# Optimization experiments

Hardware: AMD Instinct MI355X
Metric: run time of the kernel (lower is better)

The kernel has to match this reference:

```python
import jax, jax.numpy as jnp
import numpy as np

B, M, D, H = 8, 1024, 512, 8


def setup_inputs() -> dict:
    key = jax.random.key(0)
    ks = jax.random.split(key, 8)
    s = 0.02
    return {
        'x': jax.random.normal(ks[0], (B, M, D), jnp.float32),
        'scale': jnp.ones((M, D), jnp.float32),
        'Wq': jax.random.normal(ks[1], (H, D, D), jnp.float32) * s,
        'Wk': jax.random.normal(ks[2], (H, D, D), jnp.float32) * s,
        'Wv': jax.random.normal(ks[3], (H, D, D), jnp.float32) * s,
        'Wo': jax.random.normal(ks[4], (D, H * D), jnp.float32) * s,
        'bo': jnp.zeros((D,), jnp.float32),
        'Wff': jax.random.normal(ks[5], (D, D), jnp.float32) * s,
        'bff': jnp.zeros((D,), jnp.float32),
        'Wg': jax.random.normal(ks[6], (D, D), jnp.float32) * s,
        'bg': jnp.zeros((D,), jnp.float32),
        'Wl': jax.random.normal(ks[7], (D, D), jnp.float32) * s,
        'bl': jnp.zeros((D,), jnp.float32),
        'beta': jnp.ones((1,), jnp.float32),
    }


def _rope_cos_sin(m, d):
    # theta = 10000 ** (-2*(i-1)/d), faithful to the original (note the i-1 quirk)
    i = jnp.arange(d // 2, dtype=jnp.float32)
    theta = jnp.power(10000.0, -2.0 * (i - 1.0) / d)
    ang = jnp.arange(m, dtype=jnp.float32)[:, None] * theta[None, :]  # [m, d/2]
    return jnp.cos(ang), jnp.sin(ang)


def _apply_rope(t, cos, sin):
    # t: [..., m, d]; equivalent to bmm with the block-diagonal rotation matrix R[p]
    te, to = t[..., 0::2], t[..., 1::2]
    re = te * cos + to * sin
    ro = -te * sin + to * cos
    return jnp.stack([re, ro], axis=-1).reshape(t.shape)


def _rmsnorm(x, scale):
    b, m, d = x.shape
    ff_rms = jnp.sqrt(jnp.sum(x * x, axis=(1, 2))) * (m * d) ** (-0.5)  # [b]
    return scale[None, :m, :] * (x / ff_rms[:, None, None])


def reference(x, scale, Wq, Wk, Wv, Wo, bo, Wff, bff, Wg, bg, Wl, bl, beta):
    b, m, d = x.shape
    xn = _rmsnorm(x, scale)

    # per-head full-width projections (nn.Linear: y = x @ W.T)
    q = jnp.einsum('bmd,hod->hbmo', xn, Wq)  # [H,B,M,D]
    k = jnp.einsum('bmd,hod->hbmo', xn, Wk)
    v = jnp.einsum('bmd,hod->hbmo', xn, Wv)

    cos, sin = _rope_cos_sin(m, d)
    qr = _apply_rope(q, cos, sin)
    kr = _apply_rope(k, cos, sin)

    # SDPA with is_causal=False (no mask); dropout disabled (eval)
    scores = jnp.einsum('hbqd,hbkd->hbqk', qr, kr) / jnp.sqrt(jnp.float32(d))
    attn = jax.nn.softmax(scores, axis=-1)
    ctx = jnp.einsum('hbqk,hbkd->hbqd', attn, v)  # [H,B,M,D]

    cat = jnp.transpose(ctx, (1, 2, 0, 3)).reshape(b, m, -1)  # [B,M,H*D]
    attn_out = cat @ Wo.T + bo

    x2 = xn + attn_out
    x3 = _rmsnorm(x2, scale)

    h1 = x3 @ Wff.T + bff
    g = h1 @ Wg.T + bg
    sw = g * jax.nn.sigmoid(beta * g)
    ff = sw * (h1 @ Wl.T + bl)
    return x3 + ff
```

## Files before the change

kernel.cpp:

```cpp
#include <hip/hip_runtime.h>
#include <math.h>

typedef unsigned short u16;
typedef float f32x2 __attribute__((ext_vector_type(2)));
typedef float f32x4 __attribute__((ext_vector_type(4)));
typedef __bf16 bf16x8 __attribute__((ext_vector_type(8)));
typedef unsigned short u16x4 __attribute__((ext_vector_type(4)));
typedef unsigned short u16x8 __attribute__((ext_vector_type(8)));

__device__ __forceinline__ float bf2f(u16 u) {
    union { float f; unsigned int i; } v; v.i = ((unsigned int)u) << 16; return v.f;
}
__device__ __forceinline__ u16 f2bf(float f) {
    union { float f; unsigned int i; } v; v.f = f;
    unsigned int r = v.i + 0x7fffu + ((v.i >> 16) & 1u);
    return (u16)(r >> 16);
}
__device__ __forceinline__ float dpp_swap1(float v) {
    union { float f; int i; } a, b; a.f = v;
    b.i = __builtin_amdgcn_update_dpp(0, a.i, 0xB1, 0xF, 0xF, true);
    return b.f;
}

__device__ __forceinline__ void gll(const u16* g, u16* l) {
    __builtin_amdgcn_global_load_lds((const __attribute__((address_space(1))) void*)g,
                                     (__attribute__((address_space(3))) void*)l, 16, 0, 0);
}

struct EpiBF16 {
    u16* C; long zs; int ldc;
    __device__ void operator()(int z, int m, int n, float v) const {
        C[(long)z * zs + (long)m * ldc + n] = f2bf(v);
    }
};
struct EpiScale {
    u16* C; long zs; int ldc; float s;
    __device__ void operator()(int z, int m, int n, float v) const {
        C[(long)z * zs + (long)m * ldc + n] = f2bf(v * s);
    }
};
struct EpiAcc {
    float* x2;
    __device__ void operator()(int z, int m, int n, float v) const {
        x2[(long)m * 512 + n] += v;
    }
};
struct EpiBias16 {
    u16* C; const float* bias;
    __device__ void operator()(int z, int m, int n, float v) const {
        C[(long)m * 512 + n] = f2bf(v + bias[n]);
    }
};
struct EpiGL {
    u16* g; u16* l; const float* bg; const float* bl;
    __device__ void operator()(int z, int m, int n, float v) const {
        if (n < 512) g[(long)m * 512 + n] = f2bf(v + bg[n]);
        else         l[(long)m * 512 + n - 512] = f2bf(v + bl[n - 512]);
    }
};
struct EpiCtxMul {
    u16* C; const float* rs;
    __device__ void operator()(int z, int m, int n, float v) const {
        float r = __builtin_amdgcn_rcpf(rs[(long)z * 1024 + m]);
        C[(long)z * 524288 + (long)m * 512 + n] = f2bf(v * r);
    }
};

struct EpiScores {
    u16* C; float* rs; float sscale;
    __device__ float elem(int z, int m, int n, float v) const {
        float e = __expf(v * sscale);
        C[(long)z * 1048576 + (long)m * 1024 + n] = f2bf(e);
        return e;
    }
    __device__ void row(int z, int m, float p, int l15) const {
        p += __shfl_xor(p, 1, 64); p += __shfl_xor(p, 2, 64);
        p += __shfl_xor(p, 4, 64); p += __shfl_xor(p, 8, 64);
        if (l15 == 0) atomicAdd(rs + (long)z * 1024 + m, p);
    }
};
struct EpiPart {
    float* p;
    __device__ float elem(int z, int m, int n, float v) const {
        p[(long)z * 4194304 + (long)m * 512 + n] = v;
        return 0.f;
    }
    __device__ void row(int, int, float, int) const {}
};

#define RDA(S, I) (*(const bf16x8*)(lds + (S) * 8192 + (I) * 512 + aro))
#define RDB(S, J) (*(const bf16x8*)(lds + (S) * 8192 + (J) * 512 + bro))
#define MFMA_PH(JP) do { \
    __builtin_amdgcn_s_barrier(); \
    asm volatile("s_waitcnt lgkmcnt(0)" ::: "memory"); \
    __builtin_amdgcn_sched_barrier(0); \
    __builtin_amdgcn_s_setprio(1); \
    _Pragma("unroll") \
    for (int i_ = 0; i_ < 8; i_++) { \
        acc[i_][2*(JP)]   = __builtin_amdgcn_mfma_f32_16x16x32_bf16(aF[i_], bF[0], acc[i_][2*(JP)], 0, 0, 0); \
        acc[i_][2*(JP)+1] = __builtin_amdgcn_mfma_f32_16x16x32_bf16(aF[i_], bF[1], acc[i_][2*(JP)+1], 0, 0, 0); \
    } \
    __builtin_amdgcn_s_setprio(0); \
} while (0)

__launch_bounds__(512, 2)
__global__ void gemm256_qkv(const u16* __restrict__ xnb, const u16* __restrict__ Wqkv,
                            u16* __restrict__ q, u16* __restrict__ k, u16* __restrict__ vT,
                            const float* __restrict__ csT) {
    __shared__ __align__(16) u16 lds[65536];
    const int t = threadIdx.x;
    const int lane = t & 63, wave = t >> 6;
    const int wr = wave >> 2, wc = wave & 3;
    const int l15 = lane & 15, quad = lane >> 4;
    const int sr = t >> 2;
    const int scw = ((t & 3) ^ ((t >> 3) & 3)) * 8;
    u16* lA0 = lds + wave * 512 + lane * 8;
    u16* lB0 = lds + 32768 + wave * 512 + lane * 8;
    const int ap = (quad ^ ((l15 >> 1) & 3)) * 8;
    const int aro = (wr * 128 + l15) * 32 + ap;
    const int bro = 32768 + (wc * 64 + l15) * 32 + ap;
    const int bid = blockIdx.x;

    const u16 *curA, *curB, *nxtA, *nxtB;
    int cm0, cn0, cz, cmode, nm0, nn0, nz, nmode;
    auto decode = [&](int tid, const u16*& A_, const u16*& B_,
                      int& m0_, int& n0_, int& z_, int& md_) {
        if (tid > 1535) tid = 1535;
        if (tid < 1024) {
            md_ = 0; z_ = tid & 15; int rem = tid >> 4;
            m0_ = (rem >> 1) << 8; n0_ = (rem & 1) << 8;
            A_ = xnb + (long)(m0_ + sr) * 512 + scw;
            B_ = Wqkv + z_ * 262144 + (long)(n0_ + sr) * 512 + scw;
        } else {
            int v = tid - 1024; md_ = 1; z_ = v & 7; int rem = v >> 3;
            m0_ = (rem & 1) << 8; n0_ = (rem >> 1) << 8;
            A_ = Wqkv + 4194304 + z_ * 262144 + (long)(m0_ + sr) * 512 + scw;
            B_ = xnb + (long)(n0_ + sr) * 512 + scw;
        }
    };
    decode(bid, curA, curB, cm0, cn0, cz, cmode);
    decode(bid + 256, nxtA, nxtB, nm0, nn0, nz, nmode);

    auto STGA = [&](int s) {
        const u16* base = (s < 16) ? curA : nxtA;
        int c = (s < 16) ? s : s - 16;
        u16* d = lA0 + (s & 3) * 8192;
        const u16* src = base + c * 32;
        gll(src, d); gll(src + 65536, d + 4096);
    };
    auto STGB = [&](int s) {
        const u16* base = (s < 16) ? curB : nxtB;
        int c = (s < 16) ? s : s - 16;
        u16* d = lB0 + (s & 3) * 8192;
        const u16* src = base + c * 32;
        gll(src, d); gll(src + 65536, d + 4096);
    };

    STGA(0); STGB(0); STGA(1); STGB(1); STGA(2); STGB(2);
    asm volatile("s_waitcnt vmcnt(4)" ::: "memory");
    __builtin_amdgcn_s_barrier();

    for (int j = 0; j < 6; ++j) {
        f32x4 acc[8][4] = {};
        #pragma unroll
        for (int it = 0; it < 4; ++it) {
            const int sh = 3 + it * 4;
            bf16x8 aF[8], bF[2];
            #pragma unroll
            for (int i = 0; i < 8; i++) aF[i] = RDA(0, i);
            bF[0] = RDB(0, 0); bF[1] = RDB(0, 1);
            STGA(sh);
            MFMA_PH(0);
            __builtin_amdgcn_s_barrier();
            bF[0] = RDB(0, 2); bF[1] = RDB(0, 3);
            STGB(sh);
            MFMA_PH(1);
            __builtin_amdgcn_s_barrier();
            #pragma unroll
            for (int i = 0; i < 8; i++) aF[i] = RDA(1, i);
            bF[0] = RDB(1, 0); bF[1] = RDB(1, 1);
            STGA(sh + 1);
            MFMA_PH(0);
            __builtin_amdgcn_s_barrier();
            bF[0] = RDB(1, 2); bF[1] = RDB(1, 3);
            STGB(sh + 1);
            MFMA_PH(1);
            asm volatile("s_waitcnt vmcnt(4)" ::: "memory");
            __builtin_amdgcn_s_barrier();
            #pragma unroll
            for (int i = 0; i < 8; i++) aF[i] = RDA(2, i);
            bF[0] = RDB(2, 0); bF[1] = RDB(2, 1);
            STGA(sh + 2);
            MFMA_PH(0);
            __builtin_amdgcn_s_barrier();
            bF[0] = RDB(2, 2); bF[1] = RDB(2, 3);
            STGB(sh + 2);
            MFMA_PH(1);
            __builtin_amdgcn_s_barrier();
            #pragma unroll
            for (int i = 0; i < 8; i++) aF[i] = RDA(3, i);
            bF[0] = RDB(3, 0); bF[1] = RDB(3, 1);
            STGA(sh + 3);
            MFMA_PH(0);
            __builtin_amdgcn_s_barrier();
            bF[0] = RDB(3, 2); bF[1] = RDB(3, 3);
            STGB(sh + 3);
            MFMA_PH(1);
            asm volatile("s_waitcnt vmcnt(4)" ::: "memory");
            __builtin_amdgcn_s_barrier();
        }
        if (cmode == 0) {
            u16* dst = ((cz >= 8) ? k : q) + ((long)(cz & 7) << 22);
            const int odd = l15 & 1;
            #pragma unroll
            for (int i = 0; i < 8; i++)
                #pragma unroll
                for (int r = 0; r < 4; r++) {
                    int m = cm0 + wr * 128 + i * 16 + quad * 4 + r;
                    const float* cs = csT + (long)(m & 1023) * 512;
                    #pragma unroll
                    for (int jj = 0; jj < 4; jj++) {
                        int n = cn0 + wc * 64 + jj * 16 + l15;
                        float val = acc[i][jj][r];
                        float pv = dpp_swap1(val);
                        float c = cs[(n >> 1) * 2], s = cs[(n >> 1) * 2 + 1];
                        float o = odd ? (val * c - pv * s) : (val * c + pv * s);
                        dst[(long)m * 512 + n] = f2bf(o);
                    }
                }
        } else {
            #pragma unroll
            for (int i = 0; i < 8; i++)
                #pragma unroll
                for (int r = 0; r < 4; r++) {
                    int m = cm0 + wr * 128 + i * 16 + quad * 4 + r;
                    #pragma unroll
                    for (int jj = 0; jj < 4; jj++) {
                        int n = cn0 + wc * 64 + jj * 16 + l15;
                        vT[((long)cz << 22) + ((long)(n >> 10) << 19) + ((long)m << 10) + (n & 1023)]
                            = f2bf(acc[i][jj][r]);
                    }
                }
        }
        curA = nxtA; curB = nxtB; cm0 = nm0; cn0 = nn0; cz = nz; cmode = nmode;
        decode(bid + (j + 2) * 256, nxtA, nxtB, nm0, nn0, nz, nmode);
    }
    asm volatile("s_waitcnt vmcnt(0)" ::: "memory");
}

template <class Epi>
__launch_bounds__(512, 2)
__global__ void gemm256(const u16* __restrict__ A, const u16* __restrict__ B,
                        int nkh, int kssh, int lda, int ldb,
                        long aBatch, long bBatch, long aSeg, long bSeg, Epi epi) {
    __shared__ __align__(16) u16 lds[65536];
    const int t = threadIdx.x;
    const int lane = t & 63, wave = t >> 6;
    const int wr = wave >> 2, wc = wave & 3;
    const int l15 = lane & 15, quad = lane >> 4;
    const int m0 = blockIdx.x * 256, n0 = blockIdx.y * 256;
    const int z = blockIdx.z;
    const int sr = t >> 2;
    const int scw = ((t & 3) ^ ((t >> 3) & 3)) * 8;
    const u16* gA = A + (long)z * aBatch + (long)(m0 + sr) * lda + scw;
    const u16* gB = B + (long)z * bBatch + (long)(n0 + sr) * ldb + scw;
    const long a128 = 128L * lda, b128 = 128L * ldb;
    u16* lA0 = lds + wave * 512 + lane * 8;
    u16* lB0 = lds + 32768 + wave * 512 + lane * 8;
    const int kmask = (1 << kssh) - 1;

    auto STA = [&](int shp) {
        int c = shp < nkh ? shp : nkh - 1;
        const u16* s = gA + (long)(c >> kssh) * aSeg + (c & kmask) * 32;
        u16* d = lA0 + (shp & 3) * 8192;
        gll(s, d); gll(s + a128, d + 4096);
    };
    auto STB = [&](int shp) {
        int c = shp < nkh ? shp : nkh - 1;
        const u16* s = gB + (long)(c >> kssh) * bSeg + (c & kmask) * 32;
        u16* d = lB0 + (shp & 3) * 8192;
        gll(s, d); gll(s + b128, d + 4096);
    };

    const int ap = (quad ^ ((l15 >> 1) & 3)) * 8;
    const int aro = (wr * 128 + l15) * 32 + ap;
    const int bro = 32768 + (wc * 64 + l15) * 32 + ap;
    f32x4 acc[8][4] = {};

    STA(0); STB(0); STA(1); STB(1); STA(2); STB(2);
    asm volatile("s_waitcnt vmcnt(4)" ::: "memory");
    __builtin_amdgcn_s_barrier();

    const int niter = nkh >> 2;
    int sh = 3;
    for (int it = 0; it < niter; it++) {
        bf16x8 aF[8], bF[2];
        #pragma unroll
        for (int i = 0; i < 8; i++) aF[i] = RDA(0, i);
        bF[0] = RDB(0, 0); bF[1] = RDB(0, 1);
        STA(sh);
        MFMA_PH(0);
        __builtin_amdgcn_s_barrier();
        bF[0] = RDB(0, 2); bF[1] = RDB(0, 3);
        STB(sh);
        MFMA_PH(1);
        __builtin_amdgcn_s_barrier();
        #pragma unroll
        for (int i = 0; i < 8; i++) aF[i] = RDA(1, i);
        bF[0] = RDB(1, 0); bF[1] = RDB(1, 1);
        STA(sh + 1);
        MFMA_PH(0);
        __builtin_amdgcn_s_barrier();
        bF[0] = RDB(1, 2); bF[1] = RDB(1, 3);
        STB(sh + 1);
        MFMA_PH(1);
        asm volatile("s_waitcnt vmcnt(4)" ::: "memory");
        __builtin_amdgcn_s_barrier();
        #pragma unroll
        for (int i = 0; i < 8; i++) aF[i] = RDA(2, i);
        bF[0] = RDB(2, 0); bF[1] = RDB(2, 1);
        STA(sh + 2);
        MFMA_PH(0);
        __builtin_amdgcn_s_barrier();
        bF[0] = RDB(2, 2); bF[1] = RDB(2, 3);
        STB(sh + 2);
        MFMA_PH(1);
        __builtin_amdgcn_s_barrier();
        #pragma unroll
        for (int i = 0; i < 8; i++) aF[i] = RDA(3, i);
        bF[0] = RDB(3, 0); bF[1] = RDB(3, 1);
        STA(sh + 3);
        MFMA_PH(0);
        __builtin_amdgcn_s_barrier();
        bF[0] = RDB(3, 2); bF[1] = RDB(3, 3);
        STB(sh + 3);
        MFMA_PH(1);
        asm volatile("s_waitcnt vmcnt(4)" ::: "memory");
        __builtin_amdgcn_s_barrier();
        sh += 4;
    }
    asm volatile("s_waitcnt vmcnt(0)" ::: "memory");

    #pragma unroll
    for (int i = 0; i < 8; i++)
        #pragma unroll
        for (int r = 0; r < 4; r++) {
            int m = m0 + wr * 128 + i * 16 + quad * 4 + r;
            float p = 0.f;
            #pragma unroll
            for (int j = 0; j < 4; j++)
                p += epi.elem(z, m, n0 + wc * 64 + j * 16 + l15, acc[i][j][r]);
            epi.row(z, m, p, l15);
        }
}
#undef RDA
#undef RDB
#undef MFMA_PH

template <class Epi>
__launch_bounds__(256, 4)
__global__ void gemm128(const u16* __restrict__ A, const u16* __restrict__ B,
                        int Kseg, int nSeg, int lda, int ldb,
                        long aBatch, long bBatch, long aSeg, Epi epi) {
    __shared__ __align__(16) u16 sA[8192];
    __shared__ __align__(16) u16 sB[8192];
    const int t = threadIdx.x;
    const int lane = t & 63, wave = t >> 6;
    const int wr = wave >> 1, wc = wave & 1;
    const int l15 = lane & 15, quad = lane >> 4;
    const int m0 = blockIdx.x * 128, n0 = blockIdx.y * 128;
    const int sr = t >> 2;
    const int scw = ((t & 3) ^ ((t >> 3) & 3)) * 8;
    const u16* gA = A + (long)blockIdx.z * aBatch + (long)(m0 + sr) * lda + scw;
    const u16* gB = B + (long)blockIdx.z * bBatch + (long)(n0 + sr) * ldb + scw;
    const long a2 = 64L * lda, b2 = 64L * ldb;
    u16* lA = sA + wave * 512 + lane * 8;
    u16* lB = sB + wave * 512 + lane * 8;
    const int ap = (quad ^ ((l15 >> 1) & 3)) * 8;
    const int ab = (wr * 64 + l15) * 32 + ap;
    const int bb = (wc * 64 + l15) * 32 + ap;
    f32x4 acc[4][4] = {};
    for (int s = 0; s < nSeg; s++) {
        const u16* gAs = gA + (long)s * aSeg;
        const u16* gBs = gB + s * Kseg;
        for (int k0 = 0; k0 < Kseg; k0 += 64) {
            gll(gAs + k0, lA);             gll(gAs + k0 + a2, lA + 2048);
            gll(gBs + k0, lB);             gll(gBs + k0 + b2, lB + 2048);
            gll(gAs + k0 + 32, lA + 4096); gll(gAs + k0 + 32 + a2, lA + 6144);
            gll(gBs + k0 + 32, lB + 4096); gll(gBs + k0 + 32 + b2, lB + 6144);
            __syncthreads();
            #pragma unroll
            for (int half = 0; half < 2; half++) {
                bf16x8 aF[4], bF[4];
                #pragma unroll
                for (int i = 0; i < 4; i++) aF[i] = *(const bf16x8*)(sA + half * 4096 + ab + i * 512);
                #pragma unroll
                for (int j = 0; j < 4; j++) bF[j] = *(const bf16x8*)(sB + half * 4096 + bb + j * 512);
                #pragma unroll
                for (int i = 0; i < 4; i++)
                    #pragma unroll
                    for (int j = 0; j < 4; j++)
                        acc[i][j] = __builtin_amdgcn_mfma_f32_16x16x32_bf16(aF[i], bF[j], acc[i][j], 0, 0, 0);
            }
            __syncthreads();
        }
    }
    #pragma unroll
    for (int i = 0; i < 4; i++)
        #pragma unroll
        for (int j = 0; j < 4; j++)
            #pragma unroll
            for (int r = 0; r < 4; r++)
                epi(blockIdx.z, m0 + wr * 64 + i * 16 + quad * 4 + r,
                    n0 + wc * 64 + j * 16 + l15, acc[i][j][r]);
}

__device__ __forceinline__ float waveSum(float v) {
    #pragma unroll
    for (int o = 32; o > 0; o >>= 1) v += __shfl_down(v, o, 64);
    return v;
}
__device__ __forceinline__ float invFromPart(const float* part, int b) {
    float s = part[b * 64 + (threadIdx.x & 63)];
    s = waveSum(s);
    s = __shfl(s, 0, 64);
    return sqrtf(524288.0f / s);
}

__global__ void sumsq_f32(const float* __restrict__ x, float* __restrict__ part) {
    __shared__ float tmp[4];
    long base = (long)blockIdx.x * 524288 + (long)blockIdx.y * 8192;
    float s = 0.f;
    for (int i = threadIdx.x * 4; i < 8192; i += 1024) {
        f32x4 v = *(const f32x4*)(x + base + i);
        s += v[0] * v[0] + v[1] * v[1] + v[2] * v[2] + v[3] * v[3];
    }
    s = waveSum(s);
    if ((threadIdx.x & 63) == 0) tmp[threadIdx.x >> 6] = s;
    __syncthreads();
    if (threadIdx.x == 0) part[blockIdx.x * 64 + blockIdx.y] = tmp[0] + tmp[1] + tmp[2] + tmp[3];
}
__global__ void combine_x2(float* __restrict__ x2, const float* __restrict__ p,
                           float* __restrict__ part) {
    __shared__ float tmp[4];
    long base = (long)blockIdx.x * 524288 + (long)blockIdx.y * 8192;
    float s = 0.f;
    for (int i = threadIdx.x * 4; i < 8192; i += 1024) {
        f32x4 v = *(const f32x4*)(x2 + base + i);
        v = v + *(const f32x4*)(p + base + i);
        v = v + *(const f32x4*)(p + 4194304 + base + i);
        v = v + *(const f32x4*)(p + 8388608 + base + i);
        v = v + *(const f32x4*)(p + 12582912 + base + i);
        *(f32x4*)(x2 + base + i) = v;
        s += v[0] * v[0] + v[1] * v[1] + v[2] * v[2] + v[3] * v[3];
    }
    s = waveSum(s);
    if ((threadIdx.x & 63) == 0) tmp[threadIdx.x >> 6] = s;
    __syncthreads();
    if (threadIdx.x == 0) part[blockIdx.x * 64 + blockIdx.y] = tmp[0] + tmp[1] + tmp[2] + tmp[3];
}
__global__ void finalize_inv(const float* __restrict__ part, float* __restrict__ inv) {
    float s = part[blockIdx.x * 64 + threadIdx.x];
    s = waveSum(s);
    if (threadIdx.x == 0) inv[blockIdx.x] = sqrtf(524288.0f / s);
}
__global__ void rmsnorm1f_a(const float* __restrict__ x, const float* __restrict__ scale,
                            const float* __restrict__ part, const float* __restrict__ bo,
                            u16* __restrict__ xnb, float* __restrict__ x2) {
    long i = ((long)blockIdx.x * 256 + threadIdx.x) * 4;
    int b = (int)(i >> 19);
    float inv = invFromPart(part, b);
    f32x4 xv = *(const f32x4*)(x + i);
    f32x4 sv = *(const f32x4*)(scale + (int)(i & 524287));
    f32x4 bv = *(const f32x4*)(bo + (int)(i & 511));
    f32x4 v; u16x4 o;
    #pragma unroll
    for (int j = 0; j < 4; j++) { v[j] = xv[j] * inv * sv[j]; o[j] = f2bf(v[j]); }
    *(u16x4*)(xnb + i) = o;
    *(f32x4*)(x2 + i) = v + bv;
}
__global__ void rmsnorm2_a(const float* __restrict__ x2, const float* __restrict__ scale,
                           const float* __restrict__ part, u16* __restrict__ x3b) {
    long i = ((long)blockIdx.x * 256 + threadIdx.x) * 4;
    int b = (int)(i >> 19);
    float inv = invFromPart(part, b);
    f32x4 xv = *(const f32x4*)(x2 + i);
    f32x4 sv = *(const f32x4*)(scale + (int)(i & 524287));
    u16x4 o;
    #pragma unroll
    for (int j = 0; j < 4; j++) o[j] = f2bf(xv[j] * inv * sv[j]);
    *(u16x4*)(x3b + i) = o;
}
__global__ void final_out_a(const float* __restrict__ x2, const float* __restrict__ scale,
                            const float* __restrict__ part, const u16* __restrict__ g,
                            const u16* __restrict__ l, const float* __restrict__ beta,
                            float* __restrict__ out) {
    long i = ((long)blockIdx.x * 256 + threadIdx.x) * 4;
    int b = (int)(i >> 19);
    float inv2 = invFromPart(part, b);
    float bta = beta[0];
    f32x4 xv = *(const f32x4*)(x2 + i);
    f32x4 sv = *(const f32x4*)(scale + (int)(i & 524287));
    u16x4 gv4 = *(const u16x4*)(g + i);
    u16x4 lv4 = *(const u16x4*)(l + i);
    f32x4 o;
    #pragma unroll
    for (int j = 0; j < 4; j++) {
        float x3 = xv[j] * inv2 * sv[j];
        float gv = bf2f(gv4[j]), lv = bf2f(lv4[j]);
        float sw = gv / (1.0f + __expf(-bta * gv));
        o[j] = x3 + sw * lv;
    }
    *(f32x4*)(out + i) = o;
}
__global__ void rmsnorm1f(const float* __restrict__ x, const float* __restrict__ scale,
                          const float* __restrict__ inv, const float* __restrict__ bo,
                          u16* __restrict__ xnb, float* __restrict__ x2) {
    long i = (long)blockIdx.x * 256 + threadIdx.x;
    int b = (int)(i >> 19), md = (int)(i & 524287);
    float v = x[i] * inv[b] * scale[md];
    xnb[i] = f2bf(v);
    x2[i] = v + bo[i & 511];
}
__global__ void rmsnorm2(const float* __restrict__ x2, const float* __restrict__ scale,
                         const float* __restrict__ inv, u16* __restrict__ x3b) {
    long i = (long)blockIdx.x * 256 + threadIdx.x;
    int b = (int)(i >> 19), md = (int)(i & 524287);
    x3b[i] = f2bf(x2[i] * inv[b] * scale[md]);
}
__global__ void final_out(const float* __restrict__ x2, const float* __restrict__ scale,
                          const float* __restrict__ inv2, const u16* __restrict__ g,
                          const u16* __restrict__ l, const float* __restrict__ beta,
                          float* __restrict__ out) {
    long i = (long)blockIdx.x * 256 + threadIdx.x;
    int b = (int)(i >> 19), md = (int)(i & 524287);
    float x3 = x2[i] * inv2[b] * scale[md];
    float gv = bf2f(g[i]), lv = bf2f(l[i]);
    float bta = beta[0];
    float sw = gv / (1.0f + expf(-bta * gv));
    out[i] = x3 + sw * lv;
}
#define LOG2_10000F 13.287712379549449f
__global__ void rope_tables_a(float* __restrict__ csT, float* __restrict__ rowsum) {
    int i = blockIdx.x * 256 + threadIdx.x;
    int m = i >> 8, j = i & 255;
    float theta = exp2f(LOG2_10000F * (-2.0f * ((float)j - 1.0f) / 512.0f));
    float ang = (float)m * theta;
    csT[2 * i] = cosf(ang); csT[2 * i + 1] = sinf(ang);
    if (i < 65536) rowsum[i] = 0.f;
}
__global__ void rope_tables(float* __restrict__ cosT, float* __restrict__ sinT) {
    int i = blockIdx.x * 256 + threadIdx.x;
    int m = i >> 8, j = i & 255;
    float theta = exp2f(LOG2_10000F * (-2.0f * ((float)j - 1.0f) / 512.0f));
    float ang = (float)m * theta;
    cosT[i] = cosf(ang); sinT[i] = sinf(ang);
}
__global__ void rope_apply(u16* __restrict__ tq, const float* __restrict__ cosT,
                           const float* __restrict__ sinT) {
    long i = (long)blockIdx.x * 256 + threadIdx.x;
    int j = (int)(i & 255), m = (int)((i >> 8) & 1023);
    float c = cosT[m * 256 + j], s = sinT[m * 256 + j];
    long base = i * 2;
    float te = bf2f(tq[base]), to = bf2f(tq[base + 1]);
    tq[base]     = f2bf(te * c + to * s);
    tq[base + 1] = f2bf(-te * s + to * c);
}
__global__ void transpose_v(const u16* __restrict__ v, u16* __restrict__ vT) {
    __shared__ u16 tile[32][33];
    long zb = (long)blockIdx.z * 524288;
    int mo = blockIdx.x * 32, oo = blockIdx.y * 32;
    int tx = threadIdx.x & 31, ty = threadIdx.x >> 5;
    for (int r = ty; r < 32; r += 8) tile[r][tx] = v[zb + (long)(mo + r) * 512 + oo + tx];
    __syncthreads();
    for (int r = ty; r < 32; r += 8) vT[zb + (long)(oo + r) * 1024 + mo + tx] = tile[tx][r];
}
__launch_bounds__(256)
__global__ void softmax_rows4(u16* __restrict__ sc) {
    int row = blockIdx.x * 4 + (threadIdx.x >> 6);
    int lane = threadIdx.x & 63;
    u16* p = sc + (long)row * 1024 + lane * 16;
    float v[16]; float mx = -1e30f;
    #pragma unroll
    for (int i = 0; i < 16; i++) { v[i] = bf2f(p[i]); mx = fmaxf(mx, v[i]); }
    #pragma unroll
    for (int o = 32; o > 0; o >>= 1) mx = fmaxf(mx, __shfl_xor(mx, o, 64));
    float s = 0.f;
    #pragma unroll
    for (int i = 0; i < 16; i++) { v[i] = expf(v[i] - mx); s += v[i]; }
    #pragma unroll
    for (int o = 32; o > 0; o >>= 1) s += __shfl_xor(s, o, 64);
    float r = 1.0f / s;
    #pragma unroll
    for (int i = 0; i < 16; i++) p[i] = f2bf(v[i] * r);
}
__device__ __forceinline__ void cvt8(const float* __restrict__ s, u16* __restrict__ d) {
    f32x4 a = *(const f32x4*)s, b = *(const f32x4*)(s + 4);
    u16x8 o;
    o[0] = f2bf(a[0]); o[1] = f2bf(a[1]); o[2] = f2bf(a[2]); o[3] = f2bf(a[3]);
    o[4] = f2bf(b[0]); o[5] = f2bf(b[1]); o[6] = f2bf(b[2]); o[7] = f2bf(b[3]);
    *(u16x8*)d = o;
}
__global__ void prep_w(const float* __restrict__ Wq, const float* __restrict__ Wk,
                       const float* __restrict__ Wv, const float* __restrict__ Wo,
                       const float* __restrict__ Wff, const float* __restrict__ Wg,
                       const float* __restrict__ Wl,
                       u16* __restrict__ Wqkvb, u16* __restrict__ Wob,
                       u16* __restrict__ Wffb, u16* __restrict__ Wglb) {
    long i = ((long)blockIdx.x * 256 + threadIdx.x) * 8;
    if (i < 2097152)      cvt8(Wq + i, Wqkvb + i);
    else if (i < 4194304) cvt8(Wk + (i - 2097152), Wqkvb + i);
    else if (i < 6291456) cvt8(Wv + (i - 4194304), Wqkvb + i);
    else if (i < 8388608) cvt8(Wo + (i - 6291456), Wob + (i - 6291456));
    else if (i < 8650752) cvt8(Wff + (i - 8388608), Wffb + (i - 8388608));
    else if (i < 8912896) cvt8(Wg + (i - 8650752), Wglb + (i - 8650752));
    else                  cvt8(Wl + (i - 8912896), Wglb + 262144 + (i - 8912896));
}
__global__ void convert_f2b(const float* __restrict__ s, u16* __restrict__ d, int n) {
    int i = blockIdx.x * 256 + threadIdx.x;
    if (i < n) d[i] = f2bf(s[i]);
}
__global__ void convert3(const float* __restrict__ a, const float* __restrict__ b,
                         const float* __restrict__ c, u16* __restrict__ d) {
    int i = blockIdx.x * 256 + threadIdx.x;
    const float* s = (i < 262144) ? a : (i < 524288) ? b : c;
    d[i] = f2bf(s[i & 262143]);
}

#define MB 1048576L
extern "C" void kernel_launch(void* const* d_in, const int* in_sizes, int n_in,
                              void* d_out, int out_size, void* d_ws, size_t ws_size,
                              hipStream_t stream) {
    (void)in_sizes; (void)n_in; (void)out_size;
    const float* x    = (const float*)d_in[0];
    const float* scale= (const float*)d_in[1];
    const float* Wq   = (const float*)d_in[2];
    const float* Wk   = (const float*)d_in[3];
    const float* Wv   = (const float*)d_in[4];
    const float* Wo   = (const float*)d_in[5];
    const float* bo   = (const float*)d_in[6];
    const float* Wff  = (const float*)d_in[7];
    const float* bff  = (const float*)d_in[8];
    const float* Wg   = (const float*)d_in[9];
    const float* bg   = (const float*)d_in[10];
    const float* Wl   = (const float*)d_in[11];
    const float* bl   = (const float*)d_in[12];
    const float* beta = (const float*)d_in[13];
    float* out = (float*)d_out;
    char* ws = (char*)d_ws;
    const float sscale = 0.044194173824159216f;

    if (ws_size >= 260000000UL) {
        u16*   xnb   = (u16*)  (ws);
        u16*   q_all = (u16*)  (ws + 8*MB);
        u16*   k_all = (u16*)  (ws + 72*MB);
        u16*   vT_all= (u16*)  (ws + 136*MB);
        u16*   sc    = (u16*)  (ws + 200*MB);
        u16*   Wqkvb = (u16*)  (ws + 200*MB);
        u16*   Wob   = (u16*)  (ws + 232*MB);
        u16*   Wffb  = (u16*)  (ws + 236*MB);
        u16*   Wglb  = (u16*)  (ws + 236*MB + 524288L);
        float* csT   = (float*)(ws + 237*MB + 1572864L);
        float* rowsum= (float*)(ws + 239*MB + 1572864L);
        float* part  = (float*)(ws + 239*MB + 1835008L);
        float* x2    = out;
        float* wop   = (float*)k_all;
        u16* x3b = k_all; u16* h1 = k_all + 4194304; u16* g = k_all + 8388608; u16* l = k_all + 12582912;

        sumsq_f32<<<dim3(8, 64), 256, 0, stream>>>(x, part);
        rmsnorm1f_a<<<4096, 256, 0, stream>>>(x, scale, part, bo, xnb, x2);
        rope_tables_a<<<1024, 256, 0, stream>>>(csT, rowsum);
        prep_w<<<4480, 256, 0, stream>>>(Wq, Wk, Wv, Wo, Wff, Wg, Wl,
                                         Wqkvb, Wob, Wffb, Wglb);

        gemm256_qkv<<<256, 512, 0, stream>>>(xnb, Wqkvb, q_all, k_all, vT_all, csT);

        for (int h0 = 0; h0 < 8; h0 += 2) {
            const long off = (long)h0 * 4194304;
            float* rsc = rowsum + (long)h0 * 8192;
            gemm256<<<dim3(4, 4, 16), 512, 0, stream>>>(q_all + off, k_all + off, 16, 4, 512, 512,
                524288L, 524288L, 512L, 512L, EpiScores{sc, rsc, sscale});
            gemm128<<<dim3(8, 4, 16), 256, 0, stream>>>(sc, vT_all + off, 1024, 1, 1024, 1024,
                1048576L, 524288L, 0L, EpiCtxMul{q_all + off, rsc});
        }
        gemm256<<<dim3(32, 2, 4), 512, 0, stream>>>(q_all, Wob, 32, 4, 512, 4096,
            8388608L, 1024L, 4194304L, 512L, EpiPart{wop});
        combine_x2<<<dim3(8, 64), 256, 0, stream>>>(x2, wop, part);
        rmsnorm2_a<<<4096, 256, 0, stream>>>(x2, scale, part, x3b);

        gemm128<<<dim3(64, 4, 1), 256, 0, stream>>>(x3b, Wffb, 512, 1, 512, 512,
            0L, 0L, 0L, EpiBias16{h1, bff});
        gemm128<<<dim3(64, 8, 1), 256, 0, stream>>>(h1, Wglb, 512, 1, 512, 512,
            0L, 0L, 0L, EpiGL{g, l, bg, bl});
        final_out_a<<<4096, 256, 0, stream>>>(x2, scale, part, g, l, beta, out);
        return;
    }

    u16*   xnb  = (u16*)  (ws);
    float* x2   = (float*)(ws + 8388608L);
    u16*   qh   = (u16*)  (ws + 25165824L);
    u16*   kh   = (u16*)  (ws + 33554432L);
    u16*   vhc  = (u16*)  (ws + 41943040L);
    u16*   vT   = (u16*)  (ws + 50331648L);
    u16*   Whb  = (u16*)  (ws + 58720256L);
    u16*   Wob  = (u16*)  (ws + 60293120L);
    u16*   Wfb  = (u16*)  (ws + 64487424L);
    u16*   Wgb  = (u16*)  (ws + 65011712L);
    u16*   Wlb  = (u16*)  (ws + 65536000L);
    float* cosT = (float*)(ws + 66060288L);
    float* sinT = (float*)(ws + 67108864L);
    float* part = (float*)(ws + 68157440L);
    float* inv1 = (float*)(ws + 68159488L);
    float* inv2 = (float*)(ws + 68159552L);
    u16*   sc   = (u16*)  (ws + 68159616L);
    u16*   x3b = qh;  u16* h1 = kh;  u16* g = vhc;  u16* l = vT;
    const bool big = ws_size >= 85002240UL;

    sumsq_f32<<<dim3(8, 64), 256, 0, stream>>>(x, part);
    finalize_inv<<<8, 64, 0, stream>>>(part, inv1);
    rmsnorm1f<<<16384, 256, 0, stream>>>(x, scale, inv1, bo, xnb, x2);
    rope_tables<<<1024, 256, 0, stream>>>(cosT, sinT);
    convert_f2b<<<8192, 256, 0, stream>>>(Wo, Wob, 2097152);
    convert_f2b<<<1024, 256, 0, stream>>>(Wff, Wfb, 262144);
    convert_f2b<<<1024, 256, 0, stream>>>(Wg, Wgb, 262144);
    convert_f2b<<<1024, 256, 0, stream>>>(Wl, Wlb, 262144);

    for (int h = 0; h < 8; h++) {
        convert3<<<3072, 256, 0, stream>>>(Wq + (long)h * 262144, Wk + (long)h * 262144,
                                           Wv + (long)h * 262144, Whb);
        gemm128<<<dim3(64, 4, 3), 256, 0, stream>>>(xnb, Whb, 512, 1, 512, 512, 0L, 262144L, 0L,
                                                    EpiBF16{qh, 4194304L, 512});
        rope_apply<<<16384, 256, 0, stream>>>(qh, cosT, sinT);
        transpose_v<<<dim3(32, 16, 8), 256, 0, stream>>>(vhc, vT);
        if (big) {
            gemm128<<<dim3(8, 8, 8), 256, 0, stream>>>(qh, kh, 512, 1, 512, 512, 524288L, 524288L,
                                                       0L, EpiScale{sc, 1048576L, 1024, sscale});
            softmax_rows4<<<2048, 256, 0, stream>>>(sc);
            gemm128<<<dim3(8, 4, 8), 256, 0, stream>>>(sc, vT, 1024, 1, 1024, 1024, 1048576L,
                                                       524288L, 0L, EpiBF16{vhc, 524288L, 512});
        } else {
            for (int b = 0; b < 8; b++) {
                gemm128<<<dim3(8, 8, 1), 256, 0, stream>>>(qh + (long)b * 524288, kh + (long)b * 524288,
                                                           512, 1, 512, 512, 0L, 0L, 0L,
                                                           EpiScale{sc, 0L, 1024, sscale});
                softmax_rows4<<<256, 256, 0, stream>>>(sc);
                gemm128<<<dim3(8, 4, 1), 256, 0, stream>>>(sc, vT + (long)b * 524288, 1024, 1, 1024,
                                                           1024, 0L, 0L, 0L,
                                                           EpiBF16{vhc + (long)b * 524288, 0L, 512});
            }
        }
        gemm128<<<dim3(64, 4, 1), 256, 0, stream>>>(vhc, Wob + (long)h * 512, 512, 1, 512, 4096,
                                                    0L, 0L, 0L, EpiAcc{x2});
    }

    sumsq_f32<<<dim3(8, 64), 256, 0, stream>>>(x2, part);
    finalize_inv<<<8, 64, 0, stream>>>(part, inv2);
    rmsnorm2<<<16384, 256, 0, stream>>>(x2, scale, inv2, x3b);
    gemm128<<<dim3(64, 4, 1), 256, 0, stream>>>(x3b, Wfb, 512, 1, 512, 512, 0L, 0L, 0L,
                                                EpiBias16{h1, bff});
    gemm128<<<dim3(64, 4, 1), 256, 0, stream>>>(h1, Wgb, 512, 1, 512, 512, 0L, 0L, 0L,
                                                EpiBias16{g, bg});
    gemm128<<<dim3(64, 4, 1), 256, 0, stream>>>(h1, Wlb, 512, 1, 512, 512, 0L, 0L, 0L,
                                                EpiBias16{l, bl});
    final_out<<<16384, 256, 0, stream>>>(x2, scale, inv2, g, l, beta, out);
}
```

Measured before the change: 610.2 us.

## Fuse scores, softmax and PV into a single flash-style attention kernel

Replaces the per-head-pair loop of a scores GEMM (writing exp'd bf16 scores to global memory) followed by a PV GEMM with one fused kernel per 128-query tile. Exponentiated scores stay in LDS and row sums are accumulated in shared memory, so the large score tensor never round-trips through HBM and seven launches disappear. In exchange the kernel has only 512 blocks with no double buffering, uses plain syncthreads between loads and MFMAs, and recomputes Q loads for each key tile. It keeps the max-free softmax (exp without subtracting the row max), which the original path also relied on.

After: 791.7 us. 29.7% more time.

```diff
diff --git a/kernel.cpp b/kernel.cpp
--- a/kernel.cpp
+++ b/kernel.cpp
@@ -58,27 +58,7 @@
         else         l[(long)m * 512 + n - 512] = f2bf(v + bl[n - 512]);
     }
 };
-struct EpiCtxMul {
-    u16* C; const float* rs;
-    __device__ void operator()(int z, int m, int n, float v) const {
-        float r = __builtin_amdgcn_rcpf(rs[(long)z * 1024 + m]);
-        C[(long)z * 524288 + (long)m * 512 + n] = f2bf(v * r);
-    }
-};
-
-struct EpiScores {
-    u16* C; float* rs; float sscale;
-    __device__ float elem(int z, int m, int n, float v) const {
-        float e = __expf(v * sscale);
-        C[(long)z * 1048576 + (long)m * 1024 + n] = f2bf(e);
-        return e;
-    }
-    __device__ void row(int z, int m, float p, int l15) const {
-        p += __shfl_xor(p, 1, 64); p += __shfl_xor(p, 2, 64);
-        p += __shfl_xor(p, 4, 64); p += __shfl_xor(p, 8, 64);
-        if (l15 == 0) atomicAdd(rs + (long)z * 1024 + m, p);
-    }
-};
+
 struct EpiPart {
     float* p;
     __device__ float elem(int z, int m, int n, float v) const {
@@ -247,6 +227,127 @@
     }
     asm volatile("s_waitcnt vmcnt(0)" ::: "memory");
 }
+
+#define PB 24576
+__launch_bounds__(512, 2)
+__global__ void fattn(u16* __restrict__ q, const u16* __restrict__ k,
+                      const u16* __restrict__ vT, float sscale) {
+    __shared__ __align__(16) u16 lds[57344];
+    __shared__ float rsum[128];
+    const int t = threadIdx.x;
+    const int lane = t & 63, wave = t >> 6;
+    const int wr = wave >> 2, wc = wave & 3;
+    const int l15 = lane & 15, quad = lane >> 4;
+    const int q0 = blockIdx.x * 128;
+    const long zb = (long)blockIdx.y * 524288;
+    const int scw = ((t & 3) ^ ((t >> 3) & 3)) * 8;
+    const int sr = t >> 2;
+    u16* st = lds + t * 8;
+    const int ap = (quad ^ ((l15 >> 1) & 3)) * 8;
+    const int abS = (wr * 64 + l15) * 32 + ap;
+    const int bbS = 8192 + (wc * 64 + l15) * 32 + ap;
+    const int abP = PB + (wr * 64 + l15) * 32 + ap;
+
+    const u16* gQ = q + zb + (long)(q0 + sr) * 512 + scw;
+    const u16* gK = k + zb + (long)sr * 512 + scw;
+    const u16* gV = vT + zb + (long)sr * 1024 + scw;
+
+    if (t < 128) rsum[t] = 0.f;
+
+    f32x4 accO[2][4][4] = {};
+    for (int kt = 0; kt < 4; kt++) {
+        const int ktb = kt * 256;
+        f32x4 accS[4][4] = {};
+        for (int k0 = 0; k0 < 512; k0 += 64) {
+            const u16* gKt = gK + (long)ktb * 512 + k0;
+            gll(gQ + k0, st);
+            gll(gQ + k0 + 32, st + 4096);
+            gll(gKt, st + 8192);
+            gll(gKt + 65536, st + 12288);
+            gll(gKt + 32, st + 16384);
+            gll(gKt + 32 + 65536, st + 20480);
+            __syncthreads();
+            #pragma unroll
+            for (int h = 0; h < 2; h++) {
+                bf16x8 aF[4], bF[4];
+                #pragma unroll
+                for (int i = 0; i < 4; i++)
+                    aF[i] = *(const bf16x8*)(lds + h * 4096 + abS + i * 512);
+                #pragma unroll
+                for (int j = 0; j < 4; j++)
+                    bF[j] = *(const bf16x8*)(lds + h * 8192 + bbS + j * 512);
+                #pragma unroll
+                for (int i = 0; i < 4; i++)
+                    #pragma unroll
+                    for (int j = 0; j < 4; j++)
+                        accS[i][j] = __builtin_amdgcn_mfma_f32_16x16x32_bf16(aF[i], bF[j], accS[i][j], 0, 0, 0);
+            }
+            __syncthreads();
+        }
+        #pragma unroll
+        for (int i = 0; i < 4; i++)
+            #pragma unroll
+            for (int r = 0; r < 4; r++) {
+                int qr = wr * 64 + i * 16 + quad * 4 + r;
+                float p = 0.f;
+                #pragma unroll
+                for (int j = 0; j < 4; j++) {
+                    int kl = wc * 64 + j * 16 + l15;
+                    float e = __expf(accS[i][j][r] * sscale);
+                    p += e;
+                    lds[PB + (kl >> 5) * 4096 + qr * 32
+                        + ((((kl >> 3) & 3) ^ ((qr >> 1) & 3)) * 8) + (kl & 7)] = f2bf(e);
+                }
+                p += __shfl_xor(p, 1, 64); p += __shfl_xor(p, 2, 64);
+                p += __shfl_xor(p, 4, 64); p += __shfl_xor(p, 8, 64);
+                if (l15 == 0) atomicAdd(&rsum[qr], p);
+            }
+        __syncthreads();
+        #pragma unroll
+        for (int dh = 0; dh < 2; dh++) {
+            const u16* gVd = gV + (long)(dh * 256) * 1024 + ktb;
+            for (int kk = 0; kk < 256; kk += 64) {
+                gll(gVd + kk, st + 8192);
+                gll(gVd + kk + 131072, st + 12288);
+                gll(gVd + kk + 32, st + 16384);
+                gll(gVd + kk + 32 + 131072, st + 20480);
+                __syncthreads();
+                #pragma unroll
+                for (int h = 0; h < 2; h++) {
+                    const int s = (kk >> 5) + h;
+                    bf16x8 aF[4], bF[4];
+                    #pragma unroll
+                    for (int i = 0; i < 4; i++)
+                        aF[i] = *(const bf16x8*)(lds + s * 4096 + abP + i * 512);
+                    #pragma unroll
+                    for (int j = 0; j < 4; j++)
+                        bF[j] = *(const bf16x8*)(lds + h * 8192 + bbS + j * 512);
+                    #pragma unroll
+                    for (int i = 0; i < 4; i++)
+                        #pragma unroll
+                        for (int j = 0; j < 4; j++)
+                            accO[dh][i][j] = __builtin_amdgcn_mfma_f32_16x16x32_bf16(aF[i], bF[j], accO[dh][i][j], 0, 0, 0);
+                }
+                __syncthreads();
+            }
+        }
+    }
+    __syncthreads();
+    #pragma unroll
+    for (int i = 0; i < 4; i++)
+        #pragma unroll
+        for (int r = 0; r < 4; r++) {
+            int qr = wr * 64 + i * 16 + quad * 4 + r;
+            float rv = __builtin_amdgcn_rcpf(rsum[qr]);
+            u16* row = q + zb + (long)(q0 + qr) * 512;
+            #pragma unroll
+            for (int dh = 0; dh < 2; dh++)
+                #pragma unroll
+                for (int j = 0; j < 4; j++)
+                    row[dh * 256 + wc * 64 + j * 16 + l15] = f2bf(accO[dh][i][j][r] * rv);
+        }
+}
+#undef PB
 
 template <class Epi>
 __launch_bounds__(512, 2)
@@ -655,7 +756,6 @@
         u16*   q_all = (u16*)  (ws + 8*MB);
         u16*   k_all = (u16*)  (ws + 72*MB);
         u16*   vT_all= (u16*)  (ws + 136*MB);
-        u16*   sc    = (u16*)  (ws + 200*MB);
         u16*   Wqkvb = (u16*)  (ws + 200*MB);
         u16*   Wob   = (u16*)  (ws + 232*MB);
         u16*   Wffb  = (u16*)  (ws + 236*MB);
@@ -675,14 +775,8 @@
 
         gemm256_qkv<<<256, 512, 0, stream>>>(xnb, Wqkvb, q_all, k_all, vT_all, csT);
 
-        for (int h0 = 0; h0 < 8; h0 += 2) {
-            const long off = (long)h0 * 4194304;
-            float* rsc = rowsum + (long)h0 * 8192;
-            gemm256<<<dim3(4, 4, 16), 512, 0, stream>>>(q_all + off, k_all + off, 16, 4, 512, 512,
-                524288L, 524288L, 512L, 512L, EpiScores{sc, rsc, sscale});
-            gemm128<<<dim3(8, 4, 16), 256, 0, stream>>>(sc, vT_all + off, 1024, 1, 1024, 1024,
-                1048576L, 524288L, 0L, EpiCtxMul{q_all + off, rsc});
-        }
+        fattn<<<dim3(8, 64), 512, 0, stream>>>(q_all, k_all, vT_all, sscale);
+
         gemm256<<<dim3(32, 2, 4), 512, 0, stream>>>(q_all, Wob, 32, 4, 512, 4096,
             8388608L, 1024L, 4194304L, 512L, EpiPart{wop});
         combine_x2<<<dim3(8, 64), 256, 0, stream>>>(x2, wop, part);
```
